# Optimization experiments

Measured on AMD Instinct MI355X. Metric: run time of the kernel, lower is better.

Reference implementation:

```python
import math
import jax, jax.numpy as jnp
import numpy as np

N, M = 2048, 128            # fine grid points, coarse points
IN_NF, H, LMAX = 256, 128, 2
A2B = 1.88973
MIN_STD = 0.32 * A2B / 2.0  # two stddevs reach min covalent radius (Bohr)
MAX_STD = 2.32 * A2B / 2.0


def _sph_lmax2(d):
    # norm-normalized real spherical harmonics (e3nn convention), unit input d[..., 3]
    x, y, z = d[..., 0], d[..., 1], d[..., 2]
    s3 = math.sqrt(3.0)
    sh0 = jnp.ones_like(x)[..., None]                                    # [., 1]
    sh1 = jnp.stack([x, y, z], axis=-1)                                  # [., 3]
    sh2 = jnp.stack([s3 * x * z, s3 * x * y,
                     y * y - 0.5 * (x * x + z * z),
                     s3 * y * z, 0.5 * s3 * (z * z - x * x)], axis=-1)   # [., 5]
    return [sh0, sh1, sh2]


def _radial(dist, nb):
    # Gaussian radial basis; two stddevs span [MIN_COV_RAD, MAX_COV_RAD]
    s = jnp.linspace(MIN_STD, MAX_STD, nb, dtype=dist.dtype)
    temps = 2.0 * s * s
    x2 = dist[..., None] ** 2
    return jnp.exp(-x2 / temps) * (2.0 / 3.0) * x2 / temps / (math.pi * temps) ** 1.5


def setup_inputs():
    key = jax.random.key(0)
    k = jax.random.split(key, 10)
    xav = math.sqrt(6.0 / (H + H))
    return {
        'h': jax.random.normal(k[0], (N, IN_NF), jnp.float32),
        'grid_coords': jax.random.normal(k[1], (N, 3), jnp.float32),
        'coarse_coords': jax.random.normal(k[2], (M, 3), jnp.float32),
        'grid_weights': jax.random.uniform(k[3], (N,), jnp.float32),
        'W_pre': jax.random.normal(k[4], (IN_NF, H), jnp.float32) * math.sqrt(2.0 / (IN_NF + H)),
        'b_pre': jnp.zeros((H,), jnp.float32),
        'W_down': jax.random.uniform(k[5], (LMAX + 1, H, H), jnp.float32, -xav, xav),
        'W_up': jax.random.uniform(k[6], (LMAX + 1, H, H), jnp.float32, -xav, xav),
        'W_post': jax.random.normal(k[7], (H, H), jnp.float32) * math.sqrt(2.0 / (H + H)),
        'b_post': jnp.zeros((H,), jnp.float32),
    }


def reference(h, grid_coords, coarse_coords, grid_weights,
              W_pre, b_pre, W_down, W_up, W_post, b_post):
    h = jax.nn.silu(h @ W_pre + b_pre)                            # [N, H]
    # all-pairs directions/distances (vect_cdist); radius_cutoff = inf -> every pair is an edge
    dvec = grid_coords[:, None, :] - coarse_coords[None, :, :]    # [N, M, 3]
    dist = jnp.sqrt((dvec * dvec + 1e-20).sum(-1))                # [N, M]
    dirs = dvec / dist[..., None]
    sh = _sph_lmax2(dirs)                                         # list of [N, M, 2l+1]
    rad = _radial(dist, H)                                        # [N, M, H]
    # tp_down: paths (0e x le -> le); l=0 uses the scalar branch (no 1/sqrt(2l+1))
    # radial gating per hidden channel + quadrature integration onto coarse nodes
    coarse = []
    for l in range(LMAX + 1):
        norm = 1.0 if l == 0 else math.sqrt(2 * l + 1)
        c = jnp.einsum('nu,uw,nmj,nmw,n->mwj',
                       h, W_down[l], sh[l], rad, grid_weights) / norm
        coarse.append(c)                                          # [M, H, 2l+1]
    # tp_up: paths (le x le -> 0e); l>0 branch divides by sqrt(2l+1); scatter back to grid
    out = 0.0
    for l in range(LMAX + 1):
        norm = 1.0 if l == 0 else math.sqrt(2 * l + 1)
        out = out + jnp.einsum('mui,uw,nmi->nw', coarse[l], W_up[l], sh[l]) / norm
    return jax.nn.silu(out @ W_post + b_post)                     # [N, H]
```

## Files before the change

kernel.cpp:

```cpp
#include <hip/hip_runtime.h>
#include <math.h>

#define N_PTS 2048
#define M_PTS 128
#define INNF  256
#define H     128

#define MIN_STDC 0.30235680f
#define MAX_STDC 2.19208680f
#define PI_F     3.14159265358979f
#define LOG2E_F  1.44269504089f

static __device__ __forceinline__ float silu_f(float x) {
  return x / (1.0f + __expf(-x));
}

__global__ __launch_bounds__(256) void k_pre(const float* __restrict__ h,
    const float* __restrict__ W_pre, const float* __restrict__ b_pre,
    const float* __restrict__ W_down, const float* __restrict__ gw,
    float* __restrict__ hdg4) {
  __shared__ float bigW[12288];
  __shared__ float h_t[8 * INNF];
  __shared__ float hp_t[8 * H];
  int t = threadIdx.x;
  int n0 = blockIdx.x * 8;
  int lw = t & 31;
  int g  = t >> 5;
  int w0 = lw * 4;

  #pragma unroll
  for (int i = 0; i < 2; ++i) {
    int idx = t + i * 256;
    int row = idx >> 6, col = (idx & 63) << 2;
    *(float4*)&h_t[row * INNF + col] =
        *(const float4*)(h + (size_t)(n0 + row) * INNF + col);
  }

  float acc[4] = {};
  for (int kc = 0; kc < 256; kc += 64) {
    __syncthreads();
    #pragma unroll
    for (int i = 0; i < 8; ++i) {
      int idx = t + i * 256;
      *(float4*)&bigW[idx * 4] = *(const float4*)(W_pre + (size_t)kc * H + idx * 4);
    }
    __syncthreads();
    #pragma unroll 4
    for (int u4 = 0; u4 < 16; ++u4) {
      float4 hv = *(const float4*)&h_t[g * INNF + kc + u4 * 4];
      float hvv[4] = {hv.x, hv.y, hv.z, hv.w};
      #pragma unroll
      for (int uu = 0; uu < 4; ++uu) {
        float4 wv = *(const float4*)&bigW[(u4 * 4 + uu) * H + w0];
        acc[0] += hvv[uu] * wv.x; acc[1] += hvv[uu] * wv.y;
        acc[2] += hvv[uu] * wv.z; acc[3] += hvv[uu] * wv.w;
      }
    }
  }
  {
    float4 bv = *(const float4*)(b_pre + w0);
    float4 o = make_float4(silu_f(acc[0] + bv.x), silu_f(acc[1] + bv.y),
                           silu_f(acc[2] + bv.z), silu_f(acc[3] + bv.w));
    __syncthreads();
    *(float4*)&hp_t[g * H + w0] = o;
  }

  float acc2[3][4] = {};
  for (int kc = 0; kc < 128; kc += 32) {
    __syncthreads();
    #pragma unroll
    for (int i = 0; i < 12; ++i) {
      int idx = t + i * 256;
      int l = idx >> 10, r4 = idx & 1023;
      *(float4*)&bigW[idx * 4] =
          *(const float4*)(W_down + ((size_t)l * H + kc) * H + r4 * 4);
    }
    __syncthreads();
    #pragma unroll 2
    for (int u4 = 0; u4 < 8; ++u4) {
      float4 pv = *(const float4*)&hp_t[g * H + kc + u4 * 4];
      float pvv[4] = {pv.x, pv.y, pv.z, pv.w};
      #pragma unroll
      for (int uu = 0; uu < 4; ++uu) {
        int ul = u4 * 4 + uu;
        #pragma unroll
        for (int l = 0; l < 3; ++l) {
          float4 wv = *(const float4*)&bigW[(l * 32 + ul) * H + w0];
          acc2[l][0] += pvv[uu] * wv.x; acc2[l][1] += pvv[uu] * wv.y;
          acc2[l][2] += pvv[uu] * wv.z; acc2[l][3] += pvv[uu] * wv.w;
        }
      }
    }
  }

  {
    const float stp = (MAX_STDC - MIN_STDC) / 127.0f;
    const float invn1 = 0.57735026919f, invn2 = 0.44721359550f;
    int n = n0 + g;
    float gwv = gw[n];
    #pragma unroll
    for (int i = 0; i < 4; ++i) {
      int w = w0 + i;
      float s = MIN_STDC + (float)w * stp;
      float temps = 2.0f * s * s;
      float coef = (2.0f / 3.0f) / (temps * powf(PI_F * temps, 1.5f));
      float sc = gwv * coef;
      *(float4*)(hdg4 + ((size_t)n * H + w) * 4) =
          make_float4(acc2[0][i] * sc, acc2[1][i] * sc * invn1,
                      acc2[2][i] * sc * invn2, 0.0f);
    }
  }
}

__global__ __launch_bounds__(256) void k_down(const float* __restrict__ gc,
    const float* __restrict__ cc, const float* __restrict__ hdg4,
    float* __restrict__ c_part) {
  __shared__ float sh_t[6144];
  __shared__ float red[9216];
  int t = threadIdx.x;
  int m0 = blockIdx.x * 4;
  int ss = blockIdx.y;
  int n0 = ss * 128;
  int wv = t >> 6;
  int ln = t & 63;
  int w0 = ln * 2;

  #pragma unroll
  for (int i = 0; i < 2; ++i) {
    int idx = t + i * 256;
    int n_loc = idx >> 2, m_loc = idx & 3;
    int n = n0 + n_loc, m = m0 + m_loc;
    float dx = gc[3*n]   - cc[3*m];
    float dy = gc[3*n+1] - cc[3*m+1];
    float dz = gc[3*n+2] - cc[3*m+2];
    float d2 = dx*dx + dy*dy + dz*dz + 3e-20f;
    float inv = rsqrtf(d2);
    float x = dx*inv, y = dy*inv, z = dz*inv;
    const float s3 = 1.73205080757f;
    float* dst = &sh_t[(size_t)idx * 12];
    dst[0] = 1.0f; dst[1] = x; dst[2] = y; dst[3] = z;
    dst[4] = s3*x*z; dst[5] = s3*x*y; dst[6] = y*y - 0.5f*(x*x + z*z);
    dst[7] = s3*y*z; dst[8] = 0.5f*s3*(z*z - x*x);
    dst[9] = d2; dst[10] = 0.0f; dst[11] = 0.0f;
  }
  __syncthreads();

  const float stp = (MAX_STDC - MIN_STDC) / 127.0f;
  float sA = MIN_STDC + (float)w0 * stp;
  float sB = MIN_STDC + (float)(w0 + 1) * stp;
  float cA = -LOG2E_F / (2.0f * sA * sA);
  float cB = -LOG2E_F / (2.0f * sB * sB);

  float acc[4][9][2] = {};
  for (int j = 0; j < 32; ++j) {
    int nl = wv * 32 + j;
    const float4* hb = (const float4*)(hdg4 + ((size_t)(n0 + nl) * H + w0) * 4);
    float4 hv0 = hb[0];
    float4 hv1 = hb[1];
    const float* shb = &sh_t[(size_t)nl * 48];
    #pragma unroll
    for (int mm = 0; mm < 4; ++mm) {
      float4 q0 = *(const float4*)(shb + mm*12);
      float4 q1 = *(const float4*)(shb + mm*12 + 4);
      float4 q2 = *(const float4*)(shb + mm*12 + 8);
      float e0 = exp2f(q2.y * cA);
      float e1 = exp2f(q2.y * cB);
      float rp0 = e0 * q2.y, rp1 = e1 * q2.y;
      float a00 = hv0.x*rp0, a01 = hv0.y*rp0, a02 = hv0.z*rp0;
      float a10 = hv1.x*rp1, a11 = hv1.y*rp1, a12 = hv1.z*rp1;
      acc[mm][0][0] += a00;        acc[mm][0][1] += a10;
      acc[mm][1][0] += a01*q0.y;   acc[mm][1][1] += a11*q0.y;
      acc[mm][2][0] += a01*q0.z;   acc[mm][2][1] += a11*q0.z;
      acc[mm][3][0] += a01*q0.w;   acc[mm][3][1] += a11*q0.w;
      acc[mm][4][0] += a02*q1.x;   acc[mm][4][1] += a12*q1.x;
      acc[mm][5][0] += a02*q1.y;   acc[mm][5][1] += a12*q1.y;
      acc[mm][6][0] += a02*q1.z;   acc[mm][6][1] += a12*q1.z;
      acc[mm][7][0] += a02*q1.w;   acc[mm][7][1] += a12*q1.w;
      acc[mm][8][0] += a02*q2.x;   acc[mm][8][1] += a12*q2.x;
    }
  }

  __syncthreads();
  if (wv & 1) {
    float* dst = &red[(wv >> 1) * 4608];
    #pragma unroll
    for (int mm = 0; mm < 4; ++mm)
      #pragma unroll
      for (int li = 0; li < 9; ++li)
        *(float2*)&dst[(mm*9 + li)*128 + w0] =
            make_float2(acc[mm][li][0], acc[mm][li][1]);
  }
  __syncthreads();
  if (!(wv & 1)) {
    const float* src = &red[(wv >> 1) * 4608];
    #pragma unroll
    for (int mm = 0; mm < 4; ++mm)
      #pragma unroll
      for (int li = 0; li < 9; ++li) {
        float2 v = *(const float2*)&src[(mm*9 + li)*128 + w0];
        acc[mm][li][0] += v.x; acc[mm][li][1] += v.y;
      }
  }
  __syncthreads();
  if (wv == 2) {
    #pragma unroll
    for (int mm = 0; mm < 4; ++mm)
      #pragma unroll
      for (int li = 0; li < 9; ++li)
        *(float2*)&red[(mm*9 + li)*128 + w0] =
            make_float2(acc[mm][li][0], acc[mm][li][1]);
  }
  __syncthreads();
  if (wv == 0) {
    #pragma unroll
    for (int mm = 0; mm < 4; ++mm)
      #pragma unroll
      for (int li = 0; li < 9; ++li) {
        float2 v = *(const float2*)&red[(mm*9 + li)*128 + w0];
        float2 o = make_float2(acc[mm][li][0] + v.x, acc[mm][li][1] + v.y);
        *(float2*)&c_part[(((size_t)ss*M_PTS + m0 + mm)*9 + li)*H + w0] = o;
      }
  }
}

__global__ __launch_bounds__(128) void k_cu(const float* __restrict__ c_part,
    const float* __restrict__ W_up, float* __restrict__ CU9) {
  __shared__ float c_lds[H];
  int t = threadIdx.x;
  int m = blockIdx.x, li = blockIdx.y;
  float v = 0.0f;
  #pragma unroll
  for (int s = 0; s < 16; ++s)
    v += c_part[(((size_t)s*M_PTS + m)*9 + li)*H + t];
  c_lds[t] = v;
  __syncthreads();

  int l = (li == 0) ? 0 : (li < 4 ? 1 : 2);
  const float invn[3] = {1.0f, 0.57735026919f, 0.44721359550f};
  float acc = 0.0f;
  for (int u = 0; u < H; u += 4) {
    float w0 = W_up[((size_t)l*H + u + 0)*H + t];
    float w1 = W_up[((size_t)l*H + u + 1)*H + t];
    float w2 = W_up[((size_t)l*H + u + 2)*H + t];
    float w3 = W_up[((size_t)l*H + u + 3)*H + t];
    acc += c_lds[u]*w0 + c_lds[u+1]*w1 + c_lds[u+2]*w2 + c_lds[u+3]*w3;
  }
  CU9[((size_t)m*9 + li)*H + t] = acc * invn[l];
}

__global__ __launch_bounds__(256) void k_up(const float* __restrict__ gc,
    const float* __restrict__ cc, const float* __restrict__ CU9,
    float* __restrict__ out_part) {
  __shared__ float At[72 * 36];
  __shared__ float Bl[72 * 128];
  int t = threadIdx.x;
  int n0 = blockIdx.x * 32;
  int ks = blockIdx.y;
  int wq  = t & 31;
  int tgn = t >> 5;
  int w0 = wq * 4;
  float acc[4][4] = {};

  for (int ch = 0; ch < 2; ++ch) {
    int m0 = ks*16 + ch*8;
    if (ch) __syncthreads();
    {
      int n_loc = t >> 3, mrel = t & 7;
      int n = n0 + n_loc, m = m0 + mrel;
      float dx = gc[3*n]   - cc[3*m];
      float dy = gc[3*n+1] - cc[3*m+1];
      float dz = gc[3*n+2] - cc[3*m+2];
      float d2 = dx*dx + dy*dy + dz*dz + 3e-20f;
      float inv = rsqrtf(d2);
      float x = dx*inv, y = dy*inv, z = dz*inv;
      const float s3 = 1.73205080757f;
      float sh[9];
      sh[0] = 1.0f; sh[1] = x; sh[2] = y; sh[3] = z;
      sh[4] = s3*x*z; sh[5] = s3*x*y; sh[6] = y*y - 0.5f*(x*x + z*z);
      sh[7] = s3*y*z; sh[8] = 0.5f*s3*(z*z - x*x);
      #pragma unroll
      for (int li = 0; li < 9; ++li)
        At[(mrel*9 + li)*36 + n_loc] = sh[li];
    }
    #pragma unroll
    for (int i = 0; i < 9; ++i) {
      int idx = t + i*256;
      *(float4*)&Bl[idx*4] = *(const float4*)(CU9 + (size_t)m0*9*H + idx*4);
    }
    __syncthreads();

    #pragma unroll 8
    for (int k = 0; k < 72; ++k) {
      float4 a = *(const float4*)&At[k*36 + 4*tgn];
      float4 b = *(const float4*)&Bl[k*128 + w0];
      float av[4] = {a.x, a.y, a.z, a.w};
      float bv[4] = {b.x, b.y, b.z, b.w};
      #pragma unroll
      for (int r = 0; r < 4; ++r)
        #pragma unroll
        for (int c = 0; c < 4; ++c)
          acc[r][c] += av[r] * bv[c];
    }
  }
  #pragma unroll
  for (int r = 0; r < 4; ++r) {
    size_t row = (size_t)ks*N_PTS + n0 + 4*tgn + r;
    *(float4*)(out_part + row*H + w0) =
        make_float4(acc[r][0], acc[r][1], acc[r][2], acc[r][3]);
  }
}

__global__ __launch_bounds__(256) void k_post(const float* __restrict__ out_part,
    const float* __restrict__ W_post, const float* __restrict__ b_post,
    float* __restrict__ out) {
  __shared__ float op[4 * H];
  int t = threadIdx.x;
  int n0 = blockIdx.x * 4;
  int w = t & 127, nh = t >> 7;

  #pragma unroll
  for (int i = 0; i < 2; ++i) {
    int idx = t + i*256;
    int nl = idx >> 7, ww = idx & 127;
    float v = 0.0f;
    #pragma unroll
    for (int s = 0; s < 8; ++s)
      v += out_part[((size_t)s*N_PTS + n0 + nl)*H + ww];
    op[nl*H + ww] = v;
  }
  __syncthreads();

  float acc[2] = {0.0f, 0.0f};
  for (int u = 0; u < H; u += 4) {
    float4 p0 = *(const float4*)&op[(nh*2 + 0)*H + u];
    float4 p1 = *(const float4*)&op[(nh*2 + 1)*H + u];
    float w0 = W_post[(u+0)*H + w];
    float w1 = W_post[(u+1)*H + w];
    float w2 = W_post[(u+2)*H + w];
    float w3 = W_post[(u+3)*H + w];
    acc[0] += p0.x*w0 + p0.y*w1 + p0.z*w2 + p0.w*w3;
    acc[1] += p1.x*w0 + p1.y*w1 + p1.z*w2 + p1.w*w3;
  }
  float bp = b_post[w];
  out[(size_t)(n0 + nh*2 + 0)*H + w] = silu_f(acc[0] + bp);
  out[(size_t)(n0 + nh*2 + 1)*H + w] = silu_f(acc[1] + bp);
}

extern "C" void kernel_launch(void* const* d_in, const int* in_sizes, int n_in,
                              void* d_out, int out_size, void* d_ws, size_t ws_size,
                              hipStream_t stream) {
  const float* h      = (const float*)d_in[0];
  const float* gc     = (const float*)d_in[1];
  const float* cc     = (const float*)d_in[2];
  const float* gw     = (const float*)d_in[3];
  const float* W_pre  = (const float*)d_in[4];
  const float* b_pre  = (const float*)d_in[5];
  const float* W_down = (const float*)d_in[6];
  const float* W_up   = (const float*)d_in[7];
  const float* W_post = (const float*)d_in[8];
  const float* b_post = (const float*)d_in[9];

  float* ws       = (float*)d_ws;
  float* hdg4     = ws;
  float* c_part   = hdg4 + 1048576;
  float* CU9      = c_part + 2359296;
  float* out_part = c_part;
  float* out      = (float*)d_out;

  k_pre <<<256,           256, 0, stream>>>(h, W_pre, b_pre, W_down, gw, hdg4);
  k_down<<<dim3(32,16),   256, 0, stream>>>(gc, cc, hdg4, c_part);
  k_cu  <<<dim3(128,9),   128, 0, stream>>>(c_part, W_up, CU9);
  k_up  <<<dim3(64,8),    256, 0, stream>>>(gc, cc, CU9, out_part);
  k_post<<<512,           256, 0, stream>>>(out_part, W_post, b_post, out);
}
```

Measured before the change: 138.7 us.

## Halve k_down N-chunk, double grid, share one LDS buffer for occupancy

k_down now handles 64 grid points per block instead of 128 and launches 32 N-slices, so there are twice as many blocks. The spherical-harmonic table and the reduction scratch now share one LDS array, and launch_bounds(256,4) asks for four blocks per CU. The aim is more parallelism and occupancy on the main accumulation kernel. In exchange, the partial-sum buffer doubles, k_cu must sum 32 partials instead of 16, and each block pays the fixed cross-wave reduction cost over half the work.

```diff
diff --git a/kernel.cpp b/kernel.cpp
--- a/kernel.cpp
+++ b/kernel.cpp
@@ -112,23 +112,20 @@
   }
 }
 
-__global__ __launch_bounds__(256) void k_down(const float* __restrict__ gc,
+__global__ __launch_bounds__(256, 4) void k_down(const float* __restrict__ gc,
     const float* __restrict__ cc, const float* __restrict__ hdg4,
     float* __restrict__ c_part) {
-  __shared__ float sh_t[6144];
-  __shared__ float red[9216];
+  __shared__ float lds[9216];
   int t = threadIdx.x;
   int m0 = blockIdx.x * 4;
   int ss = blockIdx.y;
-  int n0 = ss * 128;
+  int n0 = ss * 64;
   int wv = t >> 6;
   int ln = t & 63;
   int w0 = ln * 2;
 
-  #pragma unroll
-  for (int i = 0; i < 2; ++i) {
-    int idx = t + i * 256;
-    int n_loc = idx >> 2, m_loc = idx & 3;
+  {
+    int n_loc = t >> 2, m_loc = t & 3;
     int n = n0 + n_loc, m = m0 + m_loc;
     float dx = gc[3*n]   - cc[3*m];
     float dy = gc[3*n+1] - cc[3*m+1];
@@ -137,11 +134,11 @@
     float inv = rsqrtf(d2);
     float x = dx*inv, y = dy*inv, z = dz*inv;
     const float s3 = 1.73205080757f;
-    float* dst = &sh_t[(size_t)idx * 12];
-    dst[0] = 1.0f; dst[1] = x; dst[2] = y; dst[3] = z;
-    dst[4] = s3*x*z; dst[5] = s3*x*y; dst[6] = y*y - 0.5f*(x*x + z*z);
-    dst[7] = s3*y*z; dst[8] = 0.5f*s3*(z*z - x*x);
-    dst[9] = d2; dst[10] = 0.0f; dst[11] = 0.0f;
+    float* dst = &lds[(size_t)t * 12];
+    *(float4*)(dst)     = make_float4(1.0f, x, y, z);
+    *(float4*)(dst + 4) = make_float4(s3*x*z, s3*x*y,
+                                      y*y - 0.5f*(x*x + z*z), s3*y*z);
+    *(float4*)(dst + 8) = make_float4(0.5f*s3*(z*z - x*x), d2, 0.0f, 0.0f);
   }
   __syncthreads();
 
@@ -152,12 +149,12 @@
   float cB = -LOG2E_F / (2.0f * sB * sB);
 
   float acc[4][9][2] = {};
-  for (int j = 0; j < 32; ++j) {
-    int nl = wv * 32 + j;
+  for (int j = 0; j < 16; ++j) {
+    int nl = wv * 16 + j;
     const float4* hb = (const float4*)(hdg4 + ((size_t)(n0 + nl) * H + w0) * 4);
     float4 hv0 = hb[0];
     float4 hv1 = hb[1];
-    const float* shb = &sh_t[(size_t)nl * 48];
+    const float* shb = &lds[(size_t)nl * 48];
     #pragma unroll
     for (int mm = 0; mm < 4; ++mm) {
       float4 q0 = *(const float4*)(shb + mm*12);
@@ -182,7 +179,7 @@
 
   __syncthreads();
   if (wv & 1) {
-    float* dst = &red[(wv >> 1) * 4608];
+    float* dst = &lds[(wv >> 1) * 4608];
     #pragma unroll
     for (int mm = 0; mm < 4; ++mm)
       #pragma unroll
@@ -192,7 +189,7 @@
   }
   __syncthreads();
   if (!(wv & 1)) {
-    const float* src = &red[(wv >> 1) * 4608];
+    const float* src = &lds[(wv >> 1) * 4608];
     #pragma unroll
     for (int mm = 0; mm < 4; ++mm)
       #pragma unroll
@@ -207,7 +204,7 @@
     for (int mm = 0; mm < 4; ++mm)
       #pragma unroll
       for (int li = 0; li < 9; ++li)
-        *(float2*)&red[(mm*9 + li)*128 + w0] =
+        *(float2*)&lds[(mm*9 + li)*128 + w0] =
             make_float2(acc[mm][li][0], acc[mm][li][1]);
   }
   __syncthreads();
@@ -216,7 +213,7 @@
     for (int mm = 0; mm < 4; ++mm)
       #pragma unroll
       for (int li = 0; li < 9; ++li) {
-        float2 v = *(const float2*)&red[(mm*9 + li)*128 + w0];
+        float2 v = *(const float2*)&lds[(mm*9 + li)*128 + w0];
         float2 o = make_float2(acc[mm][li][0] + v.x, acc[mm][li][1] + v.y);
         *(float2*)&c_part[(((size_t)ss*M_PTS + m0 + mm)*9 + li)*H + w0] = o;
       }
@@ -230,7 +227,7 @@
   int m = blockIdx.x, li = blockIdx.y;
   float v = 0.0f;
   #pragma unroll
-  for (int s = 0; s < 16; ++s)
+  for (int s = 0; s < 32; ++s)
     v += c_part[(((size_t)s*M_PTS + m)*9 + li)*H + t];
   c_lds[t] = v;
   __syncthreads();
@@ -363,12 +360,12 @@
   float* ws       = (float*)d_ws;
   float* hdg4     = ws;
   float* c_part   = hdg4 + 1048576;
-  float* CU9      = c_part + 2359296;
+  float* CU9      = c_part + 4718592;
   float* out_part = c_part;
   float* out      = (float*)d_out;
 
   k_pre <<<256,           256, 0, stream>>>(h, W_pre, b_pre, W_down, gw, hdg4);
-  k_down<<<dim3(32,16),   256, 0, stream>>>(gc, cc, hdg4, c_part);
+  k_down<<<dim3(32,32),   256, 0, stream>>>(gc, cc, hdg4, c_part);
   k_cu  <<<dim3(128,9),   128, 0, stream>>>(c_part, W_up, CU9);
   k_up  <<<dim3(64,8),    256, 0, stream>>>(gc, cc, CU9, out_part);
   k_post<<<512,           256, 0, stream>>>(out_part, W_post, b_post, out);
```

After: 143.1 us. 1.03x slower.

## Split K across warps in k_pre with register tiling and tree reduction

Applied to the files above, without the earlier changes.

Each warp in k_pre now owns a slice of the reduction dimension and computes all 8 rows at once, so each weight float4 loaded from shared memory is reused across 8 rows instead of 1. Partial sums are combined through shared memory, with a single step for the first GEMM and a multi-stage tree for the three W_down products. This cuts shared-memory traffic per FMA. In exchange it adds extra syncs and serial reduction stages, leaves only one warp doing the final writes, and raises register pressure with 96 accumulators per thread plus 32KB more LDS.

```diff
diff --git a/kernel.cpp b/kernel.cpp
--- a/kernel.cpp
+++ b/kernel.cpp
@@ -20,13 +20,14 @@
     const float* __restrict__ W_down, const float* __restrict__ gw,
     float* __restrict__ hdg4) {
   __shared__ float bigW[12288];
+  __shared__ float red[8192];
   __shared__ float h_t[8 * INNF];
   __shared__ float hp_t[8 * H];
   int t = threadIdx.x;
   int n0 = blockIdx.x * 8;
-  int lw = t & 31;
-  int g  = t >> 5;
-  int w0 = lw * 4;
+  int wq = t & 31;
+  int kw = t >> 5;
+  int w0 = wq * 4;
 
   #pragma unroll
   for (int i = 0; i < 2; ++i) {
@@ -36,7 +37,7 @@
         *(const float4*)(h + (size_t)(n0 + row) * INNF + col);
   }
 
-  float acc[4] = {};
+  float acc[8][4] = {};
   for (int kc = 0; kc < 256; kc += 64) {
     __syncthreads();
     #pragma unroll
@@ -45,27 +46,47 @@
       *(float4*)&bigW[idx * 4] = *(const float4*)(W_pre + (size_t)kc * H + idx * 4);
     }
     __syncthreads();
-    #pragma unroll 4
-    for (int u4 = 0; u4 < 16; ++u4) {
-      float4 hv = *(const float4*)&h_t[g * INNF + kc + u4 * 4];
-      float hvv[4] = {hv.x, hv.y, hv.z, hv.w};
-      #pragma unroll
-      for (int uu = 0; uu < 4; ++uu) {
-        float4 wv = *(const float4*)&bigW[(u4 * 4 + uu) * H + w0];
-        acc[0] += hvv[uu] * wv.x; acc[1] += hvv[uu] * wv.y;
-        acc[2] += hvv[uu] * wv.z; acc[3] += hvv[uu] * wv.w;
-      }
-    }
-  }
+    #pragma unroll
+    for (int kk4 = 0; kk4 < 2; ++kk4) {
+      int kb = kw * 8 + kk4 * 4;
+      float4 hv[8];
+      #pragma unroll
+      for (int n = 0; n < 8; ++n)
+        hv[n] = *(const float4*)&h_t[n * INNF + kc + kb];
+      #pragma unroll
+      for (int kk = 0; kk < 4; ++kk) {
+        float4 wv = *(const float4*)&bigW[(kb + kk) * H + w0];
+        #pragma unroll
+        for (int n = 0; n < 8; ++n) {
+          float hval = (kk == 0) ? hv[n].x : (kk == 1) ? hv[n].y
+                     : (kk == 2) ? hv[n].z : hv[n].w;
+          acc[n][0] += hval * wv.x; acc[n][1] += hval * wv.y;
+          acc[n][2] += hval * wv.z; acc[n][3] += hval * wv.w;
+        }
+      }
+    }
+  }
+  __syncthreads();
+  #pragma unroll
+  for (int n = 0; n < 8; ++n)
+    *(float4*)&red[(kw * 8 + n) * 128 + w0] =
+        make_float4(acc[n][0], acc[n][1], acc[n][2], acc[n][3]);
+  __syncthreads();
   {
-    float4 bv = *(const float4*)(b_pre + w0);
-    float4 o = make_float4(silu_f(acc[0] + bv.x), silu_f(acc[1] + bv.y),
-                           silu_f(acc[2] + bv.z), silu_f(acc[3] + bv.w));
-    __syncthreads();
-    *(float4*)&hp_t[g * H + w0] = o;
-  }
-
-  float acc2[3][4] = {};
+    int rn = t >> 5, rw = t & 31;
+    float4 s = make_float4(0.0f, 0.0f, 0.0f, 0.0f);
+    #pragma unroll
+    for (int k2 = 0; k2 < 8; ++k2) {
+      float4 v = *(const float4*)&red[(k2 * 8 + rn) * 128 + rw * 4];
+      s.x += v.x; s.y += v.y; s.z += v.z; s.w += v.w;
+    }
+    float4 bv = *(const float4*)(b_pre + rw * 4);
+    float4 o = make_float4(silu_f(s.x + bv.x), silu_f(s.y + bv.y),
+                           silu_f(s.z + bv.z), silu_f(s.w + bv.w));
+    *(float4*)&hp_t[rn * H + rw * 4] = o;
+  }
+
+  float acc2[3][8][4] = {};
   for (int kc = 0; kc < 128; kc += 32) {
     __syncthreads();
     #pragma unroll
@@ -76,38 +97,110 @@
           *(const float4*)(W_down + ((size_t)l * H + kc) * H + r4 * 4);
     }
     __syncthreads();
-    #pragma unroll 2
-    for (int u4 = 0; u4 < 8; ++u4) {
-      float4 pv = *(const float4*)&hp_t[g * H + kc + u4 * 4];
-      float pvv[4] = {pv.x, pv.y, pv.z, pv.w};
-      #pragma unroll
-      for (int uu = 0; uu < 4; ++uu) {
-        int ul = u4 * 4 + uu;
+    {
+      int kb = kw * 4;
+      float4 hv[8];
+      #pragma unroll
+      for (int n = 0; n < 8; ++n)
+        hv[n] = *(const float4*)&hp_t[n * H + kc + kb];
+      #pragma unroll
+      for (int kk = 0; kk < 4; ++kk) {
         #pragma unroll
         for (int l = 0; l < 3; ++l) {
-          float4 wv = *(const float4*)&bigW[(l * 32 + ul) * H + w0];
-          acc2[l][0] += pvv[uu] * wv.x; acc2[l][1] += pvv[uu] * wv.y;
-          acc2[l][2] += pvv[uu] * wv.z; acc2[l][3] += pvv[uu] * wv.w;
+          float4 wv = *(const float4*)&bigW[(l * 32 + kb + kk) * H + w0];
+          #pragma unroll
+          for (int n = 0; n < 8; ++n) {
+            float hval = (kk == 0) ? hv[n].x : (kk == 1) ? hv[n].y
+                       : (kk == 2) ? hv[n].z : hv[n].w;
+            acc2[l][n][0] += hval * wv.x; acc2[l][n][1] += hval * wv.y;
+            acc2[l][n][2] += hval * wv.z; acc2[l][n][3] += hval * wv.w;
+          }
         }
       }
     }
   }
 
-  {
+  __syncthreads();
+  if (kw >= 4) {
+    int s4 = kw - 4;
+    #pragma unroll
+    for (int l = 0; l < 3; ++l)
+      #pragma unroll
+      for (int n = 0; n < 8; ++n)
+        *(float4*)&bigW[(s4 * 24 + l * 8 + n) * 128 + w0] =
+            make_float4(acc2[l][n][0], acc2[l][n][1],
+                        acc2[l][n][2], acc2[l][n][3]);
+  }
+  __syncthreads();
+  if (kw < 4) {
+    #pragma unroll
+    for (int l = 0; l < 3; ++l)
+      #pragma unroll
+      for (int n = 0; n < 8; ++n) {
+        float4 v = *(const float4*)&bigW[(kw * 24 + l * 8 + n) * 128 + w0];
+        acc2[l][n][0] += v.x; acc2[l][n][1] += v.y;
+        acc2[l][n][2] += v.z; acc2[l][n][3] += v.w;
+      }
+    if (kw >= 2) {
+      int s2 = kw - 2;
+      #pragma unroll
+      for (int l = 0; l < 3; ++l)
+        #pragma unroll
+        for (int n = 0; n < 8; ++n)
+          *(float4*)&red[(s2 * 24 + l * 8 + n) * 128 + w0] =
+              make_float4(acc2[l][n][0], acc2[l][n][1],
+                          acc2[l][n][2], acc2[l][n][3]);
+    }
+  }
+  __syncthreads();
+  if (kw < 2) {
+    #pragma unroll
+    for (int l = 0; l < 3; ++l)
+      #pragma unroll
+      for (int n = 0; n < 8; ++n) {
+        float4 v = *(const float4*)&red[(kw * 24 + l * 8 + n) * 128 + w0];
+        acc2[l][n][0] += v.x; acc2[l][n][1] += v.y;
+        acc2[l][n][2] += v.z; acc2[l][n][3] += v.w;
+      }
+    if (kw == 1) {
+      #pragma unroll
+      for (int l = 0; l < 3; ++l)
+        #pragma unroll
+        for (int n = 0; n < 8; ++n)
+          *(float4*)&bigW[(l * 8 + n) * 128 + w0] =
+              make_float4(acc2[l][n][0], acc2[l][n][1],
+                          acc2[l][n][2], acc2[l][n][3]);
+    }
+  }
+  __syncthreads();
+  if (kw == 0) {
+    #pragma unroll
+    for (int l = 0; l < 3; ++l)
+      #pragma unroll
+      for (int n = 0; n < 8; ++n) {
+        float4 v = *(const float4*)&bigW[(l * 8 + n) * 128 + w0];
+        acc2[l][n][0] += v.x; acc2[l][n][1] += v.y;
+        acc2[l][n][2] += v.z; acc2[l][n][3] += v.w;
+      }
+    float gvals[8];
+    #pragma unroll
+    for (int n = 0; n < 8; ++n)
+      gvals[n] = gw[n0 + n];
     const float stp = (MAX_STDC - MIN_STDC) / 127.0f;
     const float invn1 = 0.57735026919f, invn2 = 0.44721359550f;
-    int n = n0 + g;
-    float gwv = gw[n];
     #pragma unroll
     for (int i = 0; i < 4; ++i) {
       int w = w0 + i;
       float s = MIN_STDC + (float)w * stp;
       float temps = 2.0f * s * s;
       float coef = (2.0f / 3.0f) / (temps * powf(PI_F * temps, 1.5f));
-      float sc = gwv * coef;
-      *(float4*)(hdg4 + ((size_t)n * H + w) * 4) =
-          make_float4(acc2[0][i] * sc, acc2[1][i] * sc * invn1,
-                      acc2[2][i] * sc * invn2, 0.0f);
+      #pragma unroll
+      for (int n = 0; n < 8; ++n) {
+        float sc = gvals[n] * coef;
+        *(float4*)(hdg4 + ((size_t)(n0 + n) * H + w) * 4) =
+            make_float4(acc2[0][n][i] * sc, acc2[1][n][i] * sc * invn1,
+                        acc2[2][n][i] * sc * invn2, 0.0f);
+      }
     }
   }
 }
```

New measurement: 135.8 us (median of 2 runs). -2.1%, faster.
